# Kernel optimization log

Measured on AMD Instinct MI355X. Metric: run time of the kernel, lower is better.

The kernel has to match this reference:

```python
import jax, jax.numpy as jnp
import numpy as np

B, XD, PD, D, H = 512, 32768, 512, 64, 128  # batch, x_dim, proj_dim, latent_dim, per_dim_hidden
G1 = 1024  # gene projector hidden (hardcoded in module)


def _init(k, shape, fan_in):
    s = 1.0 / np.sqrt(fan_in)
    return jax.random.uniform(k, shape, jnp.float32, -s, s)


def setup_inputs() -> dict:
    key = jax.random.key(0)
    ks = jax.random.split(key, 16)
    return {
        "x": jax.random.normal(ks[0], (B, XD), jnp.float32),
        "z": jax.random.normal(ks[1], (B, D), jnp.float32),
        "perm": jax.random.permutation(ks[2], B).astype(jnp.int32),
        # shared gene projector
        "Wg1": _init(ks[3], (XD, G1), XD), "bg1": _init(ks[4], (G1,), XD),
        "Wg2": _init(ks[5], (G1, PD), G1), "bg2": _init(ks[6], (PD,), G1),
        # per-dimension 3-layer MLPs, stacked over D. Layer-1 weight [PD+1, H]
        # is split into the h-part Wh and the z-part Wz (last input column).
        "Wh": _init(ks[7], (D, PD, H), PD + 1),
        "Wz": _init(ks[8], (D, H), PD + 1),
        "b1": _init(ks[9], (D, H), PD + 1),
        "W2": _init(ks[10], (D, H, H), H), "b2": _init(ks[11], (D, H), H),
        "W3": _init(ks[12], (D, H), H), "b3": _init(ks[13], (D,), H),
    }


def reference(x, z, perm, Wg1, bg1, Wg2, bg2, Wh, Wz, b1, W2, b2, W3, b3):
    elu = jax.nn.elu
    # shared gene projector (eval mode: dropout = identity, no noise)
    h = elu(elu(x @ Wg1 + bg1) @ Wg2 + bg2)            # [B, PD]
    # batched layer-1 of all D per-dim nets; h-projection computed once and
    # reused for the marginal pass via permutation (h_shuffled = h[perm]).
    hWh = jnp.einsum('bp,dph->bdh', h, Wh)             # [B, D, H]
    zWz = z[:, :, None] * Wz[None]                     # [B, D, H]

    def head(a1_pre):
        a1 = elu(a1_pre)                               # [B, D, H]
        a2 = elu(jnp.einsum('bdh,dhk->bdk', a1, W2) + b2)
        return jnp.einsum('bdh,dh->bd', a2, W3) + b3   # [B, D] scalar scores

    joint_score = head(hWh + zWz + b1)                 # T(h, z_j)
    marg_score = head(hWh[perm] + zWz + b1)            # T(h_shuffled, z_j)

    emas = jnp.ones((D,), x.dtype)                     # buffer init = ones, eval: no update
    et = jnp.mean(jnp.exp(marg_score), axis=0)         # [D]
    mi = jnp.mean(joint_score, axis=0) - jnp.log(et / emas)
    return -jnp.mean(mi)
```

## Files before the change

kernel.cpp:

```cpp
#include <hip/hip_runtime.h>
#include <hip/hip_bf16.h>
#include <math.h>

#define B_  512
#define XD_ 32768
#define PD_ 512
#define D_  64
#define H_  128
#define G1_ 1024

typedef __attribute__((ext_vector_type(8))) short short8v;
typedef __attribute__((ext_vector_type(4))) float floatx4;

__device__ __forceinline__ float eluf(float v) { return v > 0.f ? v : expm1f(v); }

__device__ __forceinline__ void split8t(const float* c, short8v& h, short8v& l) {
    unsigned hu[8], lu[8];
    #pragma unroll
    for (int j = 0; j < 8; j++) {
        unsigned u = __float_as_uint(c[j]);
        hu[j] = u & 0xFFFF0000u;
        float res = c[j] - __uint_as_float(hu[j]);
        lu[j] = __float_as_uint(res);
    }
    uint4 hp, lp;
    hp.x = __builtin_amdgcn_perm(hu[1], hu[0], 0x07060302u);
    hp.y = __builtin_amdgcn_perm(hu[3], hu[2], 0x07060302u);
    hp.z = __builtin_amdgcn_perm(hu[5], hu[4], 0x07060302u);
    hp.w = __builtin_amdgcn_perm(hu[7], hu[6], 0x07060302u);
    lp.x = __builtin_amdgcn_perm(lu[1], lu[0], 0x07060302u);
    lp.y = __builtin_amdgcn_perm(lu[3], lu[2], 0x07060302u);
    lp.z = __builtin_amdgcn_perm(lu[5], lu[4], 0x07060302u);
    lp.w = __builtin_amdgcn_perm(lu[7], lu[6], 0x07060302u);
    h = __builtin_bit_cast(short8v, hp);
    l = __builtin_bit_cast(short8v, lp);
}

__global__ __launch_bounds__(256) void k_trs(const float* __restrict__ x,
                                             ushort* __restrict__ xh,
                                             ushort* __restrict__ xl) {
    const int k0 = blockIdx.x * 64;
    const int m0 = blockIdx.y * 64;
    const int t = threadIdx.x;
    const int m = t & 63;
    const int kq = t >> 6;
    #pragma unroll
    for (int i = 0; i < 2; i++) {
        int kg = kq * 2 + i;
        const float* p = x + (size_t)(m0 + m) * XD_ + k0 + kg * 8;
        float4 v0 = *(const float4*)p, v1 = *(const float4*)(p + 4);
        float c[8] = {v0.x, v0.y, v0.z, v0.w, v1.x, v1.y, v1.z, v1.w};
        short8v h, l; split8t(c, h, l);
        size_t off = ((size_t)((k0 >> 3) + kg) * B_ + m0 + m) * 8;
        *(short8v*)(xh + off) = h;
        *(short8v*)(xl + off) = l;
    }
}

__global__ __launch_bounds__(256, 2) void k_gemm1t(const ushort* __restrict__ xh,
                                                   const ushort* __restrict__ xl,
                                                   const float* __restrict__ Wg1,
                                                   float* __restrict__ part,
                                                   int KS) {
    __shared__ ushort Ah[2][4 * 128 * 8], Al[2][4 * 128 * 8];
    __shared__ ushort Bh[2][4 * 128 * 8], Bl[2][4 * 128 * 8];
    const int nt = blockIdx.x, mt = blockIdx.y, ks = blockIdx.z;
    const int t = threadIdx.x;
    const int w = t >> 6, lane = t & 63;
    const int q = lane >> 4, l15 = lane & 15;
    const int wr = w >> 1, wc = w & 1;
    const int q4 = t >> 6, pr = t & 63;
    const int k0 = ks * KS;

    const size_t aoff = (((size_t)(k0 >> 3) + q4) * B_ + mt * 128 + pr) * 8;
    const ushort* Agh = xh + aoff;
    const ushort* Agl = xl + aoff;
    const float*  Bg  = Wg1 + (size_t)(k0 + q4 * 8) * G1_ + nt * 128 + pr * 2;

    floatx4 acc[4][4];
    #pragma unroll
    for (int i = 0; i < 4; i++)
        #pragma unroll
        for (int j = 0; j < 4; j++) acc[i][j] = (floatx4){0.f, 0.f, 0.f, 0.f};

    uint4 pAh0, pAh1, pAl0, pAl1;
    float2 pb[8];

    auto loadT = [&](int kt) {
        size_t o = (size_t)kt * B_;
        pAh0 = *(const uint4*)(Agh + o);
        pAh1 = *(const uint4*)(Agh + o + 512);
        pAl0 = *(const uint4*)(Agl + o);
        pAl1 = *(const uint4*)(Agl + o + 512);
        const float* p = Bg + (size_t)kt * G1_;
        #pragma unroll
        for (int kk = 0; kk < 8; kk++) pb[kk] = *(const float2*)(p + (size_t)kk * G1_);
    };

    auto stage = [&](int buf) {
        float c0[8], c1[8];
        #pragma unroll
        for (int kk = 0; kk < 8; kk++) { c0[kk] = pb[kk].x; c1[kk] = pb[kk].y; }
        short8v bh0, bl0, bh1, bl1;
        split8t(c0, bh0, bl0); split8t(c1, bh1, bl1);
        int n0 = pr * 2;
        int i0 = (q4 * 128 + (n0 ^ q4)) * 8;
        int i1 = (q4 * 128 + ((n0 + 1) ^ q4)) * 8;
        *(short8v*)&Bh[buf][i0] = bh0; *(short8v*)&Bl[buf][i0] = bl0;
        *(short8v*)&Bh[buf][i1] = bh1; *(short8v*)&Bl[buf][i1] = bl1;
        int ia = (q4 * 128 + (pr ^ q4)) * 8;
        *(uint4*)&Ah[buf][ia] = pAh0;
        *(uint4*)&Al[buf][ia] = pAl0;
        *(uint4*)&Ah[buf][ia + 512] = pAh1;
        *(uint4*)&Al[buf][ia + 512] = pAl1;
    };

    auto mma = [&](int buf) {
        short8v af[4], alf[4], bf[4], blf[4];
        #pragma unroll
        for (int i = 0; i < 4; i++) {
            int m = wr * 64 + i * 16 + l15;
            int idx = (q * 128 + (m ^ q)) * 8;
            af[i]  = *(const short8v*)&Ah[buf][idx];
            alf[i] = *(const short8v*)&Al[buf][idx];
        }
        #pragma unroll
        for (int j = 0; j < 4; j++) {
            int n = wc * 64 + j * 16 + l15;
            int idx = (q * 128 + (n ^ q)) * 8;
            bf[j]  = *(const short8v*)&Bh[buf][idx];
            blf[j] = *(const short8v*)&Bl[buf][idx];
        }
        #pragma unroll
        for (int i = 0; i < 4; i++)
            #pragma unroll
            for (int j = 0; j < 4; j++) {
                acc[i][j] = __builtin_amdgcn_mfma_f32_16x16x32_bf16(af[i],  bf[j],  acc[i][j], 0, 0, 0);
                acc[i][j] = __builtin_amdgcn_mfma_f32_16x16x32_bf16(af[i],  blf[j], acc[i][j], 0, 0, 0);
                acc[i][j] = __builtin_amdgcn_mfma_f32_16x16x32_bf16(alf[i], bf[j],  acc[i][j], 0, 0, 0);
            }
    };

    loadT(0);
    stage(0);
    loadT(32);
    asm volatile("s_waitcnt lgkmcnt(0)" ::: "memory");
    __builtin_amdgcn_s_barrier();

    const int NT = KS >> 5;
    for (int it = 0; it < NT - 1; it++) {
        const int cur = it & 1;
        stage(cur ^ 1);
        if (it + 2 < NT) loadT((it + 2) * 32);
        mma(cur);
        asm volatile("s_waitcnt lgkmcnt(0)" ::: "memory");
        __builtin_amdgcn_s_barrier();
    }
    mma((NT - 1) & 1);

    float* P = part + (size_t)ks * (B_ * G1_) + (size_t)(mt * 128) * G1_ + nt * 128;
    #pragma unroll
    for (int i = 0; i < 4; i++)
        #pragma unroll
        for (int j = 0; j < 4; j++) {
            int col = wc * 64 + j * 16 + l15;
            #pragma unroll
            for (int r = 0; r < 4; r++) {
                int row = wr * 64 + i * 16 + q * 4 + r;
                P[(size_t)row * G1_ + col] = acc[i][j][r];
            }
        }
}

__global__ __launch_bounds__(256, 2) void k_gemm1m(const float* __restrict__ x,
                                                   const float* __restrict__ Wg1,
                                                   float* __restrict__ part,
                                                   int KS) {
    __shared__ ushort Ah[4 * 128 * 8], Al[4 * 128 * 8];
    __shared__ ushort Bh[4 * 128 * 8], Bl[4 * 128 * 8];
    const int nt = blockIdx.x, mt = blockIdx.y, ks = blockIdx.z;
    const int t = threadIdx.x;
    const int w = t >> 6, lane = t & 63;
    const int q = lane >> 4, l15 = lane & 15;
    const int wr = w >> 1, wc = w & 1;
    const int kbB = t >> 6, nb = t & 63;
    const int mA = t & 127, kbA = t >> 7;
    const int k0 = ks * KS;

    const float* Ag = x + (size_t)(mt * 128 + mA) * XD_ + k0 + kbA * 8;
    const float* Bg = Wg1 + (size_t)(k0 + kbB * 8) * G1_ + nt * 128 + nb * 2;

    floatx4 acc[4][4];
    #pragma unroll
    for (int i = 0; i < 4; i++)
        #pragma unroll
        for (int j = 0; j < 4; j++) acc[i][j] = (floatx4){0.f, 0.f, 0.f, 0.f};

    float4 pa0 = *(const float4*)(Ag);
    float4 pa1 = *(const float4*)(Ag + 4);
    float4 pa2 = *(const float4*)(Ag + 16);
    float4 pa3 = *(const float4*)(Ag + 20);
    float2 pb[8];
    #pragma unroll
    for (int kk = 0; kk < 8; kk++) pb[kk] = *(const float2*)(Bg + (size_t)kk * G1_);

    for (int kt = 0; kt < KS; kt += 32) {
        float cA0[8] = {pa0.x, pa0.y, pa0.z, pa0.w, pa1.x, pa1.y, pa1.z, pa1.w};
        float cA1[8] = {pa2.x, pa2.y, pa2.z, pa2.w, pa3.x, pa3.y, pa3.z, pa3.w};
        float c0[8], c1[8];
        #pragma unroll
        for (int kk = 0; kk < 8; kk++) { c0[kk] = pb[kk].x; c1[kk] = pb[kk].y; }
        short8v ah0, al0, ah1, al1, bh0, bl0, bh1, bl1;
        split8t(cA0, ah0, al0);
        split8t(cA1, ah1, al1);
        split8t(c0, bh0, bl0);
        split8t(c1, bh1, bl1);
        if (kt + 32 < KS) {
            pa0 = *(const float4*)(Ag + kt + 32);
            pa1 = *(const float4*)(Ag + kt + 36);
            pa2 = *(const float4*)(Ag + kt + 48);
            pa3 = *(const float4*)(Ag + kt + 52);
            const float* p = Bg + (size_t)(kt + 32) * G1_;
            #pragma unroll
            for (int kk = 0; kk < 8; kk++) pb[kk] = *(const float2*)(p + (size_t)kk * G1_);
        }
        {
            int ia0 = (kbA * 128 + (mA ^ kbA)) * 8;
            int ia1 = ((kbA + 2) * 128 + (mA ^ (kbA + 2))) * 8;
            *(short8v*)&Ah[ia0] = ah0; *(short8v*)&Al[ia0] = al0;
            *(short8v*)&Ah[ia1] = ah1; *(short8v*)&Al[ia1] = al1;
            int n0i = nb * 2;
            int i0 = (kbB * 128 + (n0i ^ kbB)) * 8;
            int i1 = (kbB * 128 + ((n0i + 1) ^ kbB)) * 8;
            *(short8v*)&Bh[i0] = bh0; *(short8v*)&Bl[i0] = bl0;
            *(short8v*)&Bh[i1] = bh1; *(short8v*)&Bl[i1] = bl1;
        }
        __syncthreads();
        short8v af[4], alf[4], bf[4], blf[4];
        #pragma unroll
        for (int i = 0; i < 4; i++) {
            int m = wr * 64 + i * 16 + l15;
            int idx = (q * 128 + (m ^ q)) * 8;
            af[i]  = *(const short8v*)&Ah[idx];
            alf[i] = *(const short8v*)&Al[idx];
        }
        #pragma unroll
        for (int j = 0; j < 4; j++) {
            int n = wc * 64 + j * 16 + l15;
            int idx = (q * 128 + (n ^ q)) * 8;
            bf[j]  = *(const short8v*)&Bh[idx];
            blf[j] = *(const short8v*)&Bl[idx];
        }
        #pragma unroll
        for (int i = 0; i < 4; i++)
            #pragma unroll
            for (int j = 0; j < 4; j++) {
                acc[i][j] = __builtin_amdgcn_mfma_f32_16x16x32_bf16(af[i],  bf[j],  acc[i][j], 0, 0, 0);
                acc[i][j] = __builtin_amdgcn_mfma_f32_16x16x32_bf16(af[i],  blf[j], acc[i][j], 0, 0, 0);
                acc[i][j] = __builtin_amdgcn_mfma_f32_16x16x32_bf16(alf[i], bf[j],  acc[i][j], 0, 0, 0);
            }
        __syncthreads();
    }
    float* P = part + (size_t)ks * (B_ * G1_) + (size_t)(mt * 128) * G1_ + nt * 128;
    #pragma unroll
    for (int i = 0; i < 4; i++)
        #pragma unroll
        for (int j = 0; j < 4; j++) {
            int col = wc * 64 + j * 16 + l15;
            #pragma unroll
            for (int r = 0; r < 4; r++) {
                int row = wr * 64 + i * 16 + q * 4 + r;
                P[(size_t)row * G1_ + col] = acc[i][j][r];
            }
        }
}

__global__ __launch_bounds__(256) void k_red1(const float* __restrict__ part,
                                              const float* __restrict__ bg1,
                                              ushort* __restrict__ Gh,
                                              ushort* __restrict__ Gl,
                                              int nparts) {
    int idx = (blockIdx.x * 256 + threadIdx.x) * 8;
    const int S = B_ * G1_;
    float c[8] = {};
    for (int k = 0; k < nparts; k++) {
        const float* p = part + (size_t)k * S + idx;
        float4 v0 = *(const float4*)p, v1 = *(const float4*)(p + 4);
        c[0] += v0.x; c[1] += v0.y; c[2] += v0.z; c[3] += v0.w;
        c[4] += v1.x; c[5] += v1.y; c[6] += v1.z; c[7] += v1.w;
    }
    int cb = idx & (G1_ - 1);
    float4 b0 = *(const float4*)(bg1 + cb), b1v = *(const float4*)(bg1 + cb + 4);
    c[0] = eluf(c[0] + b0.x); c[1] = eluf(c[1] + b0.y);
    c[2] = eluf(c[2] + b0.z); c[3] = eluf(c[3] + b0.w);
    c[4] = eluf(c[4] + b1v.x); c[5] = eluf(c[5] + b1v.y);
    c[6] = eluf(c[6] + b1v.z); c[7] = eluf(c[7] + b1v.w);
    short8v h, l; split8t(c, h, l);
    *(short8v*)(Gh + idx) = h;
    *(short8v*)(Gl + idx) = l;
}

__global__ __launch_bounds__(256, 2) void k_gemm2m(const ushort* __restrict__ Gh,
                                                   const ushort* __restrict__ Gl,
                                                   const float* __restrict__ Wg2,
                                                   float* __restrict__ part2) {
    __shared__ ushort Ah[4 * 64 * 8], Al[4 * 64 * 8];
    __shared__ ushort Bh[4 * 64 * 8], Bl[4 * 64 * 8];
    const int nt = blockIdx.x, mt = blockIdx.y, ks = blockIdx.z;
    const int t = threadIdx.x;
    const int w = t >> 6, lane = t & 63;
    const int q = lane >> 4, l15 = lane & 15;
    const int kb = (t >> 4) & 3;
    const int rb = (t & 15) | (w << 4);
    const int k0 = ks * 128;

    const int cB = t & 63, g = t >> 6;

    floatx4 acc[4];
    #pragma unroll
    for (int i = 0; i < 4; i++) acc[i] = (floatx4){0.f, 0.f, 0.f, 0.f};

    for (int kt = 0; kt < 128; kt += 32) {
        {
            const ushort* pH = Gh + (size_t)(mt * 64 + rb) * G1_ + k0 + kt + kb * 8;
            const ushort* pL = Gl + (size_t)(mt * 64 + rb) * G1_ + k0 + kt + kb * 8;
            uint4 vh = *(const uint4*)pH;
            uint4 vl = *(const uint4*)pL;
            int idx = (kb * 64 + (rb ^ kb)) * 8;
            *(uint4*)&Ah[idx] = vh;
            *(uint4*)&Al[idx] = vl;
        }
        {
            float c[8];
            const float* p = Wg2 + (size_t)(k0 + kt + g * 8) * PD_ + nt * 64 + cB;
            #pragma unroll
            for (int kk = 0; kk < 8; kk++) c[kk] = p[(size_t)kk * PD_];
            short8v h, l; split8t(c, h, l);
            int idx = (g * 64 + (cB ^ g)) * 8;
            *(short8v*)&Bh[idx] = h;
            *(short8v*)&Bl[idx] = l;
        }
        __syncthreads();
        short8v af[4], alf[4], bf, blf;
        #pragma unroll
        for (int i = 0; i < 4; i++) {
            int m = i * 16 + l15;
            int idx = (q * 64 + (m ^ q)) * 8;
            af[i]  = *(const short8v*)&Ah[idx];
            alf[i] = *(const short8v*)&Al[idx];
        }
        {
            int n = w * 16 + l15;
            int idx = (q * 64 + (n ^ q)) * 8;
            bf  = *(const short8v*)&Bh[idx];
            blf = *(const short8v*)&Bl[idx];
        }
        #pragma unroll
        for (int i = 0; i < 4; i++) {
            acc[i] = __builtin_amdgcn_mfma_f32_16x16x32_bf16(af[i],  bf,  acc[i], 0, 0, 0);
            acc[i] = __builtin_amdgcn_mfma_f32_16x16x32_bf16(af[i],  blf, acc[i], 0, 0, 0);
            acc[i] = __builtin_amdgcn_mfma_f32_16x16x32_bf16(alf[i], bf,  acc[i], 0, 0, 0);
        }
        __syncthreads();
    }
    float* P = part2 + (size_t)ks * (B_ * PD_) + (size_t)(mt * 64) * PD_ + nt * 64;
    #pragma unroll
    for (int i = 0; i < 4; i++) {
        int col = w * 16 + l15;
        #pragma unroll
        for (int r = 0; r < 4; r++) {
            int row = i * 16 + q * 4 + r;
            P[(size_t)row * PD_ + col] = acc[i][r];
        }
    }
}

__global__ __launch_bounds__(256) void k_red2(const float* __restrict__ part2,
                                              const float* __restrict__ bg2,
                                              ushort* __restrict__ hh,
                                              ushort* __restrict__ hl) {
    int idx = (blockIdx.x * 256 + threadIdx.x) * 8;
    const int S = B_ * PD_;
    float c[8] = {};
    #pragma unroll
    for (int k = 0; k < 8; k++) {
        const float* p = part2 + (size_t)k * S + idx;
        float4 v0 = *(const float4*)p, v1 = *(const float4*)(p + 4);
        c[0] += v0.x; c[1] += v0.y; c[2] += v0.z; c[3] += v0.w;
        c[4] += v1.x; c[5] += v1.y; c[6] += v1.z; c[7] += v1.w;
    }
    int cb = idx & (PD_ - 1);
    float4 b0 = *(const float4*)(bg2 + cb), b1v = *(const float4*)(bg2 + cb + 4);
    c[0] = eluf(c[0] + b0.x); c[1] = eluf(c[1] + b0.y);
    c[2] = eluf(c[2] + b0.z); c[3] = eluf(c[3] + b0.w);
    c[4] = eluf(c[4] + b1v.x); c[5] = eluf(c[5] + b1v.y);
    c[6] = eluf(c[6] + b1v.z); c[7] = eluf(c[7] + b1v.w);
    short8v h, l; split8t(c, h, l);
    *(short8v*)(hh + idx) = h;
    *(short8v*)(hl + idx) = l;
}

__global__ __launch_bounds__(256, 2) void k_hwh_t(const ushort* __restrict__ hh,
                                                  const ushort* __restrict__ hl,
                                                  const float* __restrict__ Wh,
                                                  float* __restrict__ hWh) {
    __shared__ ushort Ah[2][4 * 64 * 8], Al[2][4 * 64 * 8];
    __shared__ ushort Bh[2][4 * 128 * 8], Bl[2][4 * 128 * 8];
    const int d = blockIdx.x, mt = blockIdx.y;
    const int t = threadIdx.x;
    const int w = t >> 6, lane = t & 63;
    const int q = lane >> 4, l15 = lane & 15;
    const int kb = (t >> 4) & 3;
    const int rb = (t & 15) | (w << 4);
    const int kgB = t >> 6, pr = t & 63;

    const ushort* AgH = hh + (size_t)(mt * 64 + rb) * PD_ + kb * 8;
    const ushort* AgL = hl + (size_t)(mt * 64 + rb) * PD_ + kb * 8;
    const float* Bg = Wh + (size_t)d * (PD_ * H_) + (size_t)(kgB * 8) * H_ + pr * 2;

    floatx4 acc[4][2];
    #pragma unroll
    for (int i = 0; i < 4; i++)
        #pragma unroll
        for (int j = 0; j < 2; j++) acc[i][j] = (floatx4){0.f, 0.f, 0.f, 0.f};

    uint4 pah, pal;
    float2 pb[8];

    auto loadT = [&](int kt) {
        pah = *(const uint4*)(AgH + kt);
        pal = *(const uint4*)(AgL + kt);
        const float* p = Bg + (size_t)kt * H_;
        #pragma unroll
        for (int kk = 0; kk < 8; kk++) pb[kk] = *(const float2*)(p + (size_t)kk * H_);
    };

    auto stage = [&](int buf) {
        float c0[8], c1[8];
        #pragma unroll
        for (int kk = 0; kk < 8; kk++) { c0[kk] = pb[kk].x; c1[kk] = pb[kk].y; }
        short8v bh0, bl0, bh1, bl1;
        split8t(c0, bh0, bl0); split8t(c1, bh1, bl1);
        int n0 = pr * 2;
        int i0 = (kgB * 128 + (n0 ^ kgB)) * 8;
        int i1 = (kgB * 128 + ((n0 + 1) ^ kgB)) * 8;
        *(short8v*)&Bh[buf][i0] = bh0; *(short8v*)&Bl[buf][i0] = bl0;
        *(short8v*)&Bh[buf][i1] = bh1; *(short8v*)&Bl[buf][i1] = bl1;
        int ia = (kb * 64 + (rb ^ kb)) * 8;
        *(uint4*)&Ah[buf][ia] = pah;
        *(uint4*)&Al[buf][ia] = pal;
    };

    auto mma = [&](int buf) {
        short8v af[4], alf[4], bf[2], blf[2];
        #pragma unroll
        for (int i = 0; i < 4; i++) {
            int m = i * 16 + l15;
            int idx = (q * 64 + (m ^ q)) * 8;
            af[i]  = *(const short8v*)&Ah[buf][idx];
            alf[i] = *(const short8v*)&Al[buf][idx];
        }
        #pragma unroll
        for (int j = 0; j < 2; j++) {
            int n = w * 32 + j * 16 + l15;
            int idx = (q * 128 + (n ^ q)) * 8;
            bf[j]  = *(const short8v*)&Bh[buf][idx];
            blf[j] = *(const short8v*)&Bl[buf][idx];
        }
        #pragma unroll
        for (int i = 0; i < 4; i++)
            #pragma unroll
            for (int j = 0; j < 2; j++) {
                acc[i][j] = __builtin_amdgcn_mfma_f32_16x16x32_bf16(af[i],  bf[j],  acc[i][j], 0, 0, 0);
                acc[i][j] = __builtin_amdgcn_mfma_f32_16x16x32_bf16(af[i],  blf[j], acc[i][j], 0, 0, 0);
                acc[i][j] = __builtin_amdgcn_mfma_f32_16x16x32_bf16(alf[i], bf[j],  acc[i][j], 0, 0, 0);
            }
    };

    loadT(0);
    stage(0);
    loadT(32);
    asm volatile("s_waitcnt lgkmcnt(0)" ::: "memory");
    __builtin_amdgcn_s_barrier();

    const int NT = PD_ >> 5;
    for (int it = 0; it < NT - 1; it++) {
        const int cur = it & 1;
        stage(cur ^ 1);
        if (it + 2 < NT) loadT((it + 2) * 32);
        mma(cur);
        asm volatile("s_waitcnt lgkmcnt(0)" ::: "memory");
        __builtin_amdgcn_s_barrier();
    }
    mma((NT - 1) & 1);

    #pragma unroll
    for (int i = 0; i < 4; i++)
        #pragma unroll
        for (int j = 0; j < 2; j++) {
            int col = w * 32 + j * 16 + l15;
            #pragma unroll
            for (int r = 0; r < 4; r++) {
                int row = i * 16 + q * 4 + r;
                int b = mt * 64 + row;
                hWh[(size_t)b * (D_ * H_) + d * H_ + col] = acc[i][j][r];
            }
        }
}

__global__ __launch_bounds__(256, 2) void k_heads(const float* __restrict__ hWh,
                                                  const float* __restrict__ z,
                                                  const int* __restrict__ perm,
                                                  const float* __restrict__ Wz,
                                                  const float* __restrict__ b1,
                                                  const float* __restrict__ W2,
                                                  const float* __restrict__ b2,
                                                  const float* __restrict__ W3,
                                                  const float* __restrict__ b3,
                                                  float* __restrict__ jpart,
                                                  float* __restrict__ epart) {
    const int chunk = blockIdx.x;
    const int d = blockIdx.y;
    const int t = threadIdx.x;
    const int b0 = chunk * 64;
    __shared__ ushort A1h[16 * 64 * 8];
    __shared__ ushort A1l[16 * 64 * 8];
    __shared__ float  BS[4096];
    __shared__ float  sq[4][64];
    ushort* Bh = (ushort*)BS;
    ushort* Bl = Bh + 4096;
    float*  sred = BS;

    const int w = t >> 6, lane = t & 63;
    const int q = lane >> 4, l15 = lane & 15;
    const int kb = (t >> 4) & 3;
    const int rb = (t & 15) | (w << 4);

    const float* W2d = W2 + (size_t)d * H_ * H_;
    const float* Wzd = Wz + d * H_;
    const float* b1d = b1 + d * H_;
    const float* b2d = b2 + d * H_;
    const float* W3d = W3 + d * H_;

    float result0 = 0.f, result1 = 0.f;
    for (int pass = 0; pass < 2; pass++) {
        {
            int i = t >> 2;
            int kt = t & 3;
            int h0 = kt * 32;
            int bb = b0 + i;
            int src = (pass == 0) ? bb : perm[bb];
            float zv = z[bb * D_ + d];
            const float* hrow = hWh + (size_t)src * (D_ * H_) + d * H_;
            #pragma unroll
            for (int kq = 0; kq < 4; kq++) {
                float c[8];
                int kbase = h0 + kq * 8;
                float4 v0 = *(const float4*)(hrow + kbase);
                float4 v1 = *(const float4*)(hrow + kbase + 4);
                float4 w0 = *(const float4*)(Wzd + kbase);
                float4 w1 = *(const float4*)(Wzd + kbase + 4);
                float4 x0 = *(const float4*)(b1d + kbase);
                float4 x1 = *(const float4*)(b1d + kbase + 4);
                c[0] = eluf(v0.x + zv * w0.x + x0.x);
                c[1] = eluf(v0.y + zv * w0.y + x0.y);
                c[2] = eluf(v0.z + zv * w0.z + x0.z);
                c[3] = eluf(v0.w + zv * w0.w + x0.w);
                c[4] = eluf(v1.x + zv * w1.x + x1.x);
                c[5] = eluf(v1.y + zv * w1.y + x1.y);
                c[6] = eluf(v1.z + zv * w1.z + x1.z);
                c[7] = eluf(v1.w + zv * w1.w + x1.w);
                short8v hv, lv; split8t(c, hv, lv);
                int idx = ((kt * 4 + kq) * 64 + (i ^ kq)) * 8;
                *(short8v*)&A1h[idx] = hv;
                *(short8v*)&A1l[idx] = lv;
            }
        }
        __syncthreads();
        floatx4 acc[4][2];
        #pragma unroll
        for (int i = 0; i < 4; i++)
            #pragma unroll
            for (int j = 0; j < 2; j++) acc[i][j] = (floatx4){0.f, 0.f, 0.f, 0.f};
        for (int kt2 = 0; kt2 < 4; kt2++) {
            {
                float c0[8], c1[8];
                const float* p = W2d + (size_t)(kt2 * 32 + kb * 8) * H_ + rb * 2;
                #pragma unroll
                for (int kk = 0; kk < 8; kk++) {
                    float2 v = *(const float2*)(p + (size_t)kk * H_);
                    c0[kk] = v.x; c1[kk] = v.y;
                }
                short8v h0v, l0v, h1v, l1v;
                split8t(c0, h0v, l0v);
                split8t(c1, h1v, l1v);
                int n0i = rb * 2;
                int i0 = (kb * 128 + (n0i ^ kb)) * 8;
                int i1 = (kb * 128 + ((n0i + 1) ^ kb)) * 8;
                *(short8v*)&Bh[i0] = h0v; *(short8v*)&Bl[i0] = l0v;
                *(short8v*)&Bh[i1] = h1v; *(short8v*)&Bl[i1] = l1v;
            }
            __syncthreads();
            short8v af[4], alf[4], bf[2], blf[2];
            #pragma unroll
            for (int i = 0; i < 4; i++) {
                int m = i * 16 + l15;
                int idx = ((kt2 * 4 + q) * 64 + (m ^ q)) * 8;
                af[i]  = *(const short8v*)&A1h[idx];
                alf[i] = *(const short8v*)&A1l[idx];
            }
            #pragma unroll
            for (int j = 0; j < 2; j++) {
                int n = w * 32 + j * 16 + l15;
                int idx = (q * 128 + (n ^ q)) * 8;
                bf[j]  = *(const short8v*)&Bh[idx];
                blf[j] = *(const short8v*)&Bl[idx];
            }
            #pragma unroll
            for (int i = 0; i < 4; i++)
                #pragma unroll
                for (int j = 0; j < 2; j++) {
                    acc[i][j] = __builtin_amdgcn_mfma_f32_16x16x32_bf16(af[i],  bf[j],  acc[i][j], 0, 0, 0);
                    acc[i][j] = __builtin_amdgcn_mfma_f32_16x16x32_bf16(af[i],  blf[j], acc[i][j], 0, 0, 0);
                    acc[i][j] = __builtin_amdgcn_mfma_f32_16x16x32_bf16(alf[i], bf[j],  acc[i][j], 0, 0, 0);
                }
            __syncthreads();
        }
        #pragma unroll
        for (int i = 0; i < 4; i++) {
            #pragma unroll
            for (int r = 0; r < 4; r++) {
                int b = i * 16 + q * 4 + r;
                float s = 0.f;
                #pragma unroll
                for (int j = 0; j < 2; j++) {
                    int col = w * 32 + j * 16 + l15;
                    float a2v = eluf(acc[i][j][r] + b2d[col]);
                    s = fmaf(a2v, W3d[col], s);
                }
                sred[b * 64 + w * 16 + l15] = s;
            }
        }
        __syncthreads();
        {
            int rrow = t & 63, qd = t >> 6;
            const float4* rp = (const float4*)&sred[rrow * 64 + qd * 16];
            float ps = 0.f;
            #pragma unroll
            for (int c = 0; c < 4; c++) {
                float4 v = rp[c];
                ps += v.x + v.y + v.z + v.w;
            }
            sq[qd][rrow] = ps;
        }
        __syncthreads();
        float val = 0.f;
        if (t < 64) {
            float s = b3[d] + sq[0][t] + sq[1][t] + sq[2][t] + sq[3][t];
            val = (pass == 0) ? s : expf(s);
            #pragma unroll
            for (int off = 32; off > 0; off >>= 1)
                val += __shfl_down(val, off, 64);
        }
        if (t == 0) { if (pass == 0) result0 = val; else result1 = val; }
        __syncthreads();
    }
    if (t == 0) {
        jpart[d * 8 + chunk] = result0;
        epart[d * 8 + chunk] = result1;
    }
}

__global__ void k_final(const float* __restrict__ jpart,
                        const float* __restrict__ epart,
                        float* __restrict__ out) {
    int t = threadIdx.x;
    float mj = 0.f, me = 0.f;
    #pragma unroll
    for (int c = 0; c < 8; c++) { mj += jpart[t * 8 + c]; me += epart[t * 8 + c]; }
    mj *= (1.f / 512.f);
    me *= (1.f / 512.f);
    float mi = mj - logf(me);
    #pragma unroll
    for (int off = 32; off > 0; off >>= 1) mi += __shfl_down(mi, off, 64);
    if (t == 0) out[0] = -mi * (1.f / 64.f);
}

extern "C" void kernel_launch(void* const* d_in, const int* in_sizes, int n_in,
                              void* d_out, int out_size, void* d_ws, size_t ws_size,
                              hipStream_t stream) {
    const float* x   = (const float*)d_in[0];
    const float* z   = (const float*)d_in[1];
    const int*  perm = (const int*)d_in[2];
    const float* Wg1 = (const float*)d_in[3];
    const float* bg1 = (const float*)d_in[4];
    const float* Wg2 = (const float*)d_in[5];
    const float* bg2 = (const float*)d_in[6];
    const float* Wh  = (const float*)d_in[7];
    const float* Wz  = (const float*)d_in[8];
    const float* b1  = (const float*)d_in[9];
    const float* W2  = (const float*)d_in[10];
    const float* b2  = (const float*)d_in[11];
    const float* W3  = (const float*)d_in[12];
    const float* b3  = (const float*)d_in[13];
    float* out = (float*)d_out;

    char* base = (char*)d_ws;
    const size_t PART_SLICE = (size_t)B_ * G1_ * sizeof(float);

    const size_t NEW_NEED = 16 * PART_SLICE + 67108864ull + 2097152 + 1048576 + 4096;

    if (ws_size >= NEW_NEED) {
        float* part  = (float*)base;
        ushort* xh   = (ushort*)(base + 33554432);
        ushort* xl   = (ushort*)(base + 67108864);
        float* hWh   = (float*)base;
        float* part2 = (float*)(base + 16777216);
        ushort* Gh   = (ushort*)(base + 100663296);
        ushort* Gl   = Gh + 524288;
        ushort* hh   = (ushort*)(base + 102760448);
        ushort* hl   = hh + 262144;
        float* jpart = (float*)(base + 103809024);
        float* epart = jpart + 512;

        k_trs<<<dim3(512, 8), 256, 0, stream>>>(x, xh, xl);
        k_gemm1t<<<dim3(8, 4, 16), 256, 0, stream>>>(xh, xl, Wg1, part, XD_ / 16);
        k_red1<<<256, 256, 0, stream>>>(part, bg1, Gh, Gl, 16);
        k_gemm2m<<<dim3(8, 8, 8), 256, 0, stream>>>(Gh, Gl, Wg2, part2);
        k_red2<<<128, 256, 0, stream>>>(part2, bg2, hh, hl);
        k_hwh_t<<<dim3(64, 8), 256, 0, stream>>>(hh, hl, Wh, hWh);
        k_heads<<<dim3(8, 64), 256, 0, stream>>>(hWh, z, perm, Wz, b1, W2, b2, W3, b3,
                                                 jpart, epart);
        k_final<<<1, 64, 0, stream>>>(jpart, epart, out);
    } else {
        int nks = (ws_size >= (size_t)32 * PART_SLICE + 3145728 + 4096) ? 32 : 16;
        const int KS = XD_ / nks;
        const size_t partBytes = (size_t)nks * PART_SLICE;

        float* part  = (float*)base;
        float* hWh   = (float*)base;
        float* part2 = (float*)(base + 16777216);
        ushort* Gh   = (ushort*)(base + partBytes);
        ushort* Gl   = Gh + 524288;
        ushort* hh   = (ushort*)(base + partBytes + 2097152);
        ushort* hl   = hh + 262144;
        float* jpart = (float*)(base + partBytes + 3145728);
        float* epart = jpart + 512;

        k_gemm1m<<<dim3(8, 4, nks), 256, 0, stream>>>(x, Wg1, part, KS);
        k_red1<<<256, 256, 0, stream>>>(part, bg1, Gh, Gl, nks);
        k_gemm2m<<<dim3(8, 8, 8), 256, 0, stream>>>(Gh, Gl, Wg2, part2);
        k_red2<<<128, 256, 0, stream>>>(part2, bg2, hh, hl);
        k_hwh_t<<<dim3(64, 8), 256, 0, stream>>>(hh, hl, Wh, hWh);
        k_heads<<<dim3(8, 64), 256, 0, stream>>>(hWh, z, perm, Wz, b1, W2, b2, W3, b3,
                                                 jpart, epart);
        k_final<<<1, 64, 0, stream>>>(jpart, epart, out);
    }
}
```

Before: 422.6 us.

## Double-buffer LDS tiles in gemm2 and head kernels with register prefetch

Converts the K-loops of the second projector GEMM and the per-dim head GEMM to double-buffered shared memory. The next tile's global loads are held in registers while MFMAs run on the current buffer, and there is one barrier per iteration instead of two. This is meant to hide global load latency and cut synchronisation. It costs extra LDS and registers, and the head kernel now reuses A1h for the reduction scratch.

```diff
diff --git a/kernel.cpp b/kernel.cpp
--- a/kernel.cpp
+++ b/kernel.cpp
@@ -304,8 +304,8 @@
                                                    const ushort* __restrict__ Gl,
                                                    const float* __restrict__ Wg2,
                                                    float* __restrict__ part2) {
-    __shared__ ushort Ah[4 * 64 * 8], Al[4 * 64 * 8];
-    __shared__ ushort Bh[4 * 64 * 8], Bl[4 * 64 * 8];
+    __shared__ ushort Ah[2][4 * 64 * 8], Al[2][4 * 64 * 8];
+    __shared__ ushort Bh[2][4 * 64 * 8], Bl[2][4 * 64 * 8];
     const int nt = blockIdx.x, mt = blockIdx.y, ks = blockIdx.z;
     const int t = threadIdx.x;
     const int w = t >> 6, lane = t & 63;
@@ -313,47 +313,49 @@
     const int kb = (t >> 4) & 3;
     const int rb = (t & 15) | (w << 4);
     const int k0 = ks * 128;
-
     const int cB = t & 63, g = t >> 6;
 
     floatx4 acc[4];
     #pragma unroll
     for (int i = 0; i < 4; i++) acc[i] = (floatx4){0.f, 0.f, 0.f, 0.f};
 
-    for (int kt = 0; kt < 128; kt += 32) {
-        {
-            const ushort* pH = Gh + (size_t)(mt * 64 + rb) * G1_ + k0 + kt + kb * 8;
-            const ushort* pL = Gl + (size_t)(mt * 64 + rb) * G1_ + k0 + kt + kb * 8;
-            uint4 vh = *(const uint4*)pH;
-            uint4 vl = *(const uint4*)pL;
-            int idx = (kb * 64 + (rb ^ kb)) * 8;
-            *(uint4*)&Ah[idx] = vh;
-            *(uint4*)&Al[idx] = vl;
-        }
-        {
-            float c[8];
-            const float* p = Wg2 + (size_t)(k0 + kt + g * 8) * PD_ + nt * 64 + cB;
-            #pragma unroll
-            for (int kk = 0; kk < 8; kk++) c[kk] = p[(size_t)kk * PD_];
-            short8v h, l; split8t(c, h, l);
-            int idx = (g * 64 + (cB ^ g)) * 8;
-            *(short8v*)&Bh[idx] = h;
-            *(short8v*)&Bl[idx] = l;
-        }
-        __syncthreads();
+    uint4 pAh, pAl;
+    float cb8[8];
+
+    auto loadT = [&](int kt) {
+        const ushort* pH = Gh + (size_t)(mt * 64 + rb) * G1_ + k0 + kt + kb * 8;
+        const ushort* pL = Gl + (size_t)(mt * 64 + rb) * G1_ + k0 + kt + kb * 8;
+        pAh = *(const uint4*)pH;
+        pAl = *(const uint4*)pL;
+        const float* p = Wg2 + (size_t)(k0 + kt + g * 8) * PD_ + nt * 64 + cB;
+        #pragma unroll
+        for (int kk = 0; kk < 8; kk++) cb8[kk] = p[(size_t)kk * PD_];
+    };
+
+    auto stage = [&](int buf) {
+        int ia = (kb * 64 + (rb ^ kb)) * 8;
+        *(uint4*)&Ah[buf][ia] = pAh;
+        *(uint4*)&Al[buf][ia] = pAl;
+        short8v h, l; split8t(cb8, h, l);
+        int ib = (g * 64 + (cB ^ g)) * 8;
+        *(short8v*)&Bh[buf][ib] = h;
+        *(short8v*)&Bl[buf][ib] = l;
+    };
+
+    auto mma = [&](int buf) {
         short8v af[4], alf[4], bf, blf;
         #pragma unroll
         for (int i = 0; i < 4; i++) {
             int m = i * 16 + l15;
             int idx = (q * 64 + (m ^ q)) * 8;
-            af[i]  = *(const short8v*)&Ah[idx];
-            alf[i] = *(const short8v*)&Al[idx];
+            af[i]  = *(const short8v*)&Ah[buf][idx];
+            alf[i] = *(const short8v*)&Al[buf][idx];
         }
         {
             int n = w * 16 + l15;
             int idx = (q * 64 + (n ^ q)) * 8;
-            bf  = *(const short8v*)&Bh[idx];
-            blf = *(const short8v*)&Bl[idx];
+            bf  = *(const short8v*)&Bh[buf][idx];
+            blf = *(const short8v*)&Bl[buf][idx];
         }
         #pragma unroll
         for (int i = 0; i < 4; i++) {
@@ -361,8 +363,24 @@
             acc[i] = __builtin_amdgcn_mfma_f32_16x16x32_bf16(af[i],  blf, acc[i], 0, 0, 0);
             acc[i] = __builtin_amdgcn_mfma_f32_16x16x32_bf16(alf[i], bf,  acc[i], 0, 0, 0);
         }
-        __syncthreads();
-    }
+    };
+
+    loadT(0);
+    stage(0);
+    loadT(32);
+    asm volatile("s_waitcnt lgkmcnt(0)" ::: "memory");
+    __builtin_amdgcn_s_barrier();
+
+    for (int it = 0; it < 3; it++) {
+        const int cur = it & 1;
+        stage(cur ^ 1);
+        if (it + 2 < 4) loadT((it + 2) * 32);
+        mma(cur);
+        asm volatile("s_waitcnt lgkmcnt(0)" ::: "memory");
+        __builtin_amdgcn_s_barrier();
+    }
+    mma(1);
+
     float* P = part2 + (size_t)ks * (B_ * PD_) + (size_t)(mt * 64) * PD_ + nt * 64;
     #pragma unroll
     for (int i = 0; i < 4; i++) {
@@ -525,11 +543,10 @@
     const int b0 = chunk * 64;
     __shared__ ushort A1h[16 * 64 * 8];
     __shared__ ushort A1l[16 * 64 * 8];
-    __shared__ float  BS[4096];
+    __shared__ ushort B2h[2][4 * 128 * 8];
+    __shared__ ushort B2l[2][4 * 128 * 8];
     __shared__ float  sq[4][64];
-    ushort* Bh = (ushort*)BS;
-    ushort* Bl = Bh + 4096;
-    float*  sred = BS;
+    float* sred = (float*)A1h;
 
     const int w = t >> 6, lane = t & 63;
     const int q = lane >> 4, l15 = lane & 15;
@@ -541,6 +558,26 @@
     const float* b1d = b1 + d * H_;
     const float* b2d = b2 + d * H_;
     const float* W3d = W3 + d * H_;
+
+    float2 pbW[8];
+    auto loadW2 = [&](int kt2) {
+        const float* p = W2d + (size_t)(kt2 * 32 + kb * 8) * H_ + rb * 2;
+        #pragma unroll
+        for (int kk = 0; kk < 8; kk++) pbW[kk] = *(const float2*)(p + (size_t)kk * H_);
+    };
+    auto stageB = [&](int buf) {
+        float c0[8], c1[8];
+        #pragma unroll
+        for (int kk = 0; kk < 8; kk++) { c0[kk] = pbW[kk].x; c1[kk] = pbW[kk].y; }
+        short8v h0v, l0v, h1v, l1v;
+        split8t(c0, h0v, l0v);
+        split8t(c1, h1v, l1v);
+        int n0i = rb * 2;
+        int i0 = (kb * 128 + (n0i ^ kb)) * 8;
+        int i1 = (kb * 128 + ((n0i + 1) ^ kb)) * 8;
+        *(short8v*)&B2h[buf][i0] = h0v; *(short8v*)&B2l[buf][i0] = l0v;
+        *(short8v*)&B2h[buf][i1] = h1v; *(short8v*)&B2l[buf][i1] = l1v;
+    };
 
     float result0 = 0.f, result1 = 0.f;
     for (int pass = 0; pass < 2; pass++) {
@@ -576,31 +613,19 @@
                 *(short8v*)&A1l[idx] = lv;
             }
         }
-        __syncthreads();
+        loadW2(0);
+        stageB(0);
+        loadW2(1);
+        asm volatile("s_waitcnt lgkmcnt(0)" ::: "memory");
+        __builtin_amdgcn_s_barrier();
+
         floatx4 acc[4][2];
         #pragma unroll
         for (int i = 0; i < 4; i++)
             #pragma unroll
             for (int j = 0; j < 2; j++) acc[i][j] = (floatx4){0.f, 0.f, 0.f, 0.f};
-        for (int kt2 = 0; kt2 < 4; kt2++) {
-            {
-                float c0[8], c1[8];
-                const float* p = W2d + (size_t)(kt2 * 32 + kb * 8) * H_ + rb * 2;
-                #pragma unroll
-                for (int kk = 0; kk < 8; kk++) {
-                    float2 v = *(const float2*)(p + (size_t)kk * H_);
-                    c0[kk] = v.x; c1[kk] = v.y;
-                }
-                short8v h0v, l0v, h1v, l1v;
-                split8t(c0, h0v, l0v);
-                split8t(c1, h1v, l1v);
-                int n0i = rb * 2;
-                int i0 = (kb * 128 + (n0i ^ kb)) * 8;
-                int i1 = (kb * 128 + ((n0i + 1) ^ kb)) * 8;
-                *(short8v*)&Bh[i0] = h0v; *(short8v*)&Bl[i0] = l0v;
-                *(short8v*)&Bh[i1] = h1v; *(short8v*)&Bl[i1] = l1v;
-            }
-            __syncthreads();
+
+        auto mmaP = [&](int buf, int kt2) {
             short8v af[4], alf[4], bf[2], blf[2];
             #pragma unroll
             for (int i = 0; i < 4; i++) {
@@ -613,8 +638,8 @@
             for (int j = 0; j < 2; j++) {
                 int n = w * 32 + j * 16 + l15;
                 int idx = (q * 128 + (n ^ q)) * 8;
-                bf[j]  = *(const short8v*)&Bh[idx];
-                blf[j] = *(const short8v*)&Bl[idx];
+                bf[j]  = *(const short8v*)&B2h[buf][idx];
+                blf[j] = *(const short8v*)&B2l[buf][idx];
             }
             #pragma unroll
             for (int i = 0; i < 4; i++)
@@ -624,8 +649,19 @@
                     acc[i][j] = __builtin_amdgcn_mfma_f32_16x16x32_bf16(af[i],  blf[j], acc[i][j], 0, 0, 0);
                     acc[i][j] = __builtin_amdgcn_mfma_f32_16x16x32_bf16(alf[i], bf[j],  acc[i][j], 0, 0, 0);
                 }
-            __syncthreads();
-        }
+        };
+
+        for (int kt2 = 0; kt2 < 3; kt2++) {
+            const int cur = kt2 & 1;
+            stageB(cur ^ 1);
+            if (kt2 + 2 < 4) loadW2(kt2 + 2);
+            mmaP(cur, kt2);
+            asm volatile("s_waitcnt lgkmcnt(0)" ::: "memory");
+            __builtin_amdgcn_s_barrier();
+        }
+        mmaP(1, 3);
+        __syncthreads();
+
         #pragma unroll
         for (int i = 0; i < 4; i++) {
             #pragma unroll
```

Result: no change. 423.7 us (+0.3%).
